# Performance work log

Measured on AMD Instinct MI355X. Metric: run time of the kernel, lower is better.

## Reference

```python
import jax, jax.numpy as jnp
import numpy as np

BLANK = 36
NEG = -1e30  # stand-in for -inf that stays NaN-free under logaddexp


def _ctc_loss(logits, targets, input_lengths, target_lengths):
    """CTC loss (reduction='mean', matching torch.nn.CTCLoss semantics:
    per-sample loss divided by target_length, then mean over batch).
    logits: [B, T, C] raw scores; targets: [B*L] flattened labels (fixed L per sample).
    """
    B, T, C = logits.shape
    L = targets.shape[0] // B
    tgt = targets.reshape(B, L)
    S = 2 * L + 1  # extended label length: blank-interleaved

    # log_softmax over classes, then time-major [T, B, C]
    lp = jnp.transpose(jax.nn.log_softmax(logits, axis=-1), (1, 0, 2))

    # extended targets: [blank, t1, blank, t2, ..., blank]  -> [B, S]
    ext = jnp.full((B, S), BLANK, dtype=tgt.dtype).at[:, 1::2].set(tgt)

    # gather log-probs of extended labels: [T, B, S]
    lp_ext = lp[:, jnp.arange(B)[:, None], ext]

    # positions beyond 2*target_len are invalid
    valid = jnp.arange(S)[None, :] < (2 * target_lengths[:, None] + 1)  # [B, S]
    # skip transition s-2 -> s allowed only if ext[s] != blank and ext[s] != ext[s-2]
    skip_ok = (ext != BLANK) & jnp.concatenate(
        [jnp.zeros((B, 2), bool), ext[:, 2:] != ext[:, :-2]], axis=1)

    end_idx = 2 * target_lengths  # index of final blank; [B]

    def final_ll(alpha):
        e1 = jnp.take_along_axis(alpha, end_idx[:, None], axis=1)[:, 0]
        e2 = jnp.take_along_axis(alpha, (end_idx - 1)[:, None], axis=1)[:, 0]
        return jnp.logaddexp(e1, e2)

    # t = 0 initialization
    alpha0 = jnp.full((B, S), NEG, logits.dtype)
    alpha0 = alpha0.at[:, 0].set(lp_ext[0, :, 0]).at[:, 1].set(lp_ext[0, :, 1])
    alpha0 = jnp.where(valid, alpha0, NEG)
    final0 = jnp.where(input_lengths == 1, final_ll(alpha0), NEG)

    pad1 = jnp.full((B, 1), NEG, logits.dtype)
    pad2 = jnp.full((B, 2), NEG, logits.dtype)

    def step(carry, inp):
        alpha, final = carry
        t, lpe = inp  # lpe: [B, S]
        a1 = jnp.concatenate([pad1, alpha[:, :-1]], axis=1)
        a2 = jnp.where(skip_ok, jnp.concatenate([pad2, alpha[:, :-2]], axis=1), NEG)
        new = jnp.logaddexp(jnp.logaddexp(alpha, a1), a2) + lpe
        new = jnp.where(valid, new, NEG)
        final = jnp.where(input_lengths == t + 1, final_ll(new), final)
        return (new, final), None

    (_, final), _ = jax.lax.scan(step, (alpha0, final0),
                                 (jnp.arange(1, T), lp_ext[1:]))
    return jnp.mean(-final / target_lengths.astype(logits.dtype))


def setup_inputs() -> dict:
    key = jax.random.key(0)
    k1, k2 = jax.random.split(key)
    B, T, C, L = 2048, 256, 37, 16
    logits = jax.random.normal(k1, (B, T, C), dtype=jnp.float32)
    targets = jax.random.randint(k2, (B * L,), 0, 36, dtype=jnp.int32)  # never blank
    input_lengths = jnp.full((B,), T, dtype=jnp.int32)
    target_lengths = jnp.full((B,), L, dtype=jnp.int32)
    return {"logits": logits, "targets": targets,
            "input_lengths": input_lengths, "target_lengths": target_lengths}


def reference(logits, targets, input_lengths, target_lengths):
    return _ctc_loss(logits, targets, input_lengths, target_lengths)
```

## Files before the change

### kernel.cpp

```cpp
#include <hip/hip_runtime.h>

#define BLANK 36
#define NEG -1e30f
#define CC 37
#define LOG32 3.4657359027997265f

__device__ __forceinline__ float logaddexp_f(float a, float b) {
    float m = fmaxf(a, b);
    float d = fabsf(a - b);
    return m + __logf(1.0f + __expf(-d));
}

__global__ __launch_bounds__(256) void ctc_fused_lin_kernel(
    const float* __restrict__ logits,
    const int*   __restrict__ targets,
    const int*   __restrict__ input_lengths,
    const int*   __restrict__ target_lengths,
    float*       __restrict__ per_sample,
    int B, int T, int L)
{
    __shared__ float lds[4 * 4736];
    const int lane = threadIdx.x & 63;
    const int wib  = threadIdx.x >> 6;
    const int b    = blockIdx.x * 4 + wib;
    if (b >= B) return;

    float* X0 = lds + wib * 4736;
    float* X1 = X0 + 2368;

    const int S = 2 * L + 1;
    const int tlen_s = __builtin_amdgcn_readfirstlane(target_lengths[b]);
    const int ilen_s = __builtin_amdgcn_readfirstlane(input_lengths[b]);
    const int end_s  = 2 * tlen_s;

    int ext_s = BLANK;
    if (lane < S && (lane & 1)) ext_s = targets[b * L + (lane >> 1)];
    const int ext_sm2 = __shfl_up(ext_s, 2);
    const bool skip_ok = (lane < S) && (lane >= 2) && (ext_s != BLANK) && (ext_s != ext_sm2);
    const bool valid = lane < (2 * tlen_s + 1);

    const float4* src = (const float4*)(logits + (size_t)b * T * CC);

    float z    = 0.0f;
    float racc = 0.0f;
    float capv = NEG;

    auto ZSTEP = [&](float p, int tt) {
        float z1 = __shfl_up(z, 1);
        z1 = (lane == 0) ? 0.0f : z1;
        float z2 = __shfl_up(z, 2);
        z2 = skip_ok ? z2 : 0.0f;
        const float zn = (z + z1 + z2) * p;
        z = valid ? zn : 0.0f;
        if (ilen_s == tt + 1) {
            capv = __logf(fmaxf(z, 1e-35f)) + racc - (float)(tt + 1) * LOG32;
        }
    };

    auto RESCALE = [&]() {
        float m = z;
        #pragma unroll
        for (int o = 32; o > 0; o >>= 1) m = fmaxf(m, __shfl_xor(m, o));
        m = fmaxf(m, 1e-30f);
        z *= (1.0f / m);
        racc += __logf(m);
    };

    auto SOFTMAX = [&](float* Xn) {
        float xr[CC];
        const float* row = Xn + lane * CC;
        #pragma unroll
        for (int c2 = 0; c2 < CC; ++c2) xr[c2] = row[c2];
        float m = xr[0];
        #pragma unroll
        for (int c2 = 1; c2 < CC; ++c2) m = fmaxf(m, xr[c2]);
        float ss = 0.0f;
        #pragma unroll
        for (int c2 = 0; c2 < CC; ++c2) { xr[c2] = __expf(xr[c2] - m); ss += xr[c2]; }
        const float inv = 32.0f / ss;
        float* wrow = Xn + lane * CC;
        #pragma unroll
        for (int c2 = 0; c2 < CC; ++c2) wrow[c2] = xr[c2] * inv;
    };

    {
        float4* dst = (float4*)X0;
        #pragma unroll
        for (int k = 0; k < 9; ++k) dst[k * 64 + lane] = src[k * 64 + lane];
        if (lane < 16) dst[576 + lane] = src[576 + lane];
        __builtin_amdgcn_s_waitcnt(0);
        SOFTMAX(X0);
        __builtin_amdgcn_s_waitcnt(0);
    }

    const int NC = T >> 6;
    for (int c = 0; c < NC; ++c) {
        float* Xb = (c & 1) ? X1 : X0;
        const bool more = (c + 1 < NC);

        float4 f0 = {}, f1 = {}, f2 = {}, f3 = {}, f4 = {},
               f5 = {}, f6 = {}, f7 = {}, f8 = {}, f9 = {};
        if (more) {
            const float4* s2 = src + (size_t)(c + 1) * 592;
            f0 = s2[lane];       f1 = s2[64 + lane];  f2 = s2[128 + lane];
            f3 = s2[192 + lane]; f4 = s2[256 + lane]; f5 = s2[320 + lane];
            f6 = s2[384 + lane]; f7 = s2[448 + lane]; f8 = s2[512 + lane];
            if (lane < 16) f9 = s2[576 + lane];
        }

        const int tbase = c << 6;
        float p0 = Xb[0 * CC + ext_s];
        float p1 = Xb[1 * CC + ext_s];
        float p2 = Xb[2 * CC + ext_s];
        float p3 = Xb[3 * CC + ext_s];
        float q0, q1, q2, q3;
        int g = 0;
        if (c == 0) {
            z = (valid && lane <= 1) ? p0 : 0.0f;
            if (ilen_s == 1) capv = __logf(fmaxf(z, 1e-35f)) - LOG32;
            q0 = Xb[4 * CC + ext_s];
            q1 = Xb[5 * CC + ext_s];
            q2 = Xb[6 * CC + ext_s];
            q3 = Xb[7 * CC + ext_s];
            ZSTEP(p1, 1); ZSTEP(p2, 2); ZSTEP(p3, 3);
            p0 = q0; p1 = q1; p2 = q2; p3 = q3;
            g = 1;
        }
        for (; g < 16; ++g) {
            const int r = (g + 1) << 2;
            if (g < 15) {
                q0 = Xb[(r + 0) * CC + ext_s];
                q1 = Xb[(r + 1) * CC + ext_s];
                q2 = Xb[(r + 2) * CC + ext_s];
                q3 = Xb[(r + 3) * CC + ext_s];
            }
            const int tt = tbase + (g << 2);
            ZSTEP(p0, tt); ZSTEP(p1, tt + 1); ZSTEP(p2, tt + 2); ZSTEP(p3, tt + 3);
            p0 = q0; p1 = q1; p2 = q2; p3 = q3;
            if (g & 1) RESCALE();
        }

        if (more) {
            float* Xn = (c & 1) ? X0 : X1;
            float4* dst = (float4*)Xn;
            dst[lane] = f0;       dst[64 + lane] = f1;  dst[128 + lane] = f2;
            dst[192 + lane] = f3; dst[256 + lane] = f4; dst[320 + lane] = f5;
            dst[384 + lane] = f6; dst[448 + lane] = f7; dst[512 + lane] = f8;
            if (lane < 16) dst[576 + lane] = f9;
            __builtin_amdgcn_s_waitcnt(0);
            SOFTMAX(Xn);
            __builtin_amdgcn_s_waitcnt(0);
        }
    }

    const float e1 = __shfl(capv, end_s);
    const float e2 = __shfl(capv, end_s - 1);
    const float final_v = logaddexp_f(e1, e2);
    if (lane == 0) per_sample[b] = -final_v / (float)tlen_s;
}

__global__ __launch_bounds__(256) void lse_kernel(
    const float* __restrict__ logits, float* __restrict__ denom, int N)
{
    __shared__ float lds[256 * CC];
    const int lane = threadIdx.x & 63;
    const int wib  = threadIdx.x >> 6;
    const int wave = blockIdx.x * 4 + wib;
    const long long row0 = (long long)wave * 64;
    if (row0 >= N) return;
    const int wbase = wib * 64 * CC;
    const float4* src4 = (const float4*)(logits + row0 * CC);
    const long long n4_remaining = ((long long)N * CC - row0 * CC) / 4;
    float4* lds4 = (float4*)(lds + wbase);
    #pragma unroll
    for (int k = 0; k < 10; ++k) {
        const int idx = k * 64 + lane;
        if (idx < 592 && idx < n4_remaining) lds4[idx] = src4[idx];
    }
    __builtin_amdgcn_s_waitcnt(0);
    const long long row = row0 + lane;
    if (row >= N) return;
    const float* x = lds + wbase + lane * CC;
    float m = x[0];
    #pragma unroll
    for (int c = 1; c < CC; ++c) m = fmaxf(m, x[c]);
    float s = 0.0f;
    #pragma unroll
    for (int c = 0; c < CC; ++c) s += __expf(x[c] - m);
    denom[row] = m + __logf(s);
}

__global__ __launch_bounds__(256) void ctc_alpha2_kernel(
    const float* __restrict__ logits, const float* __restrict__ denom,
    const int* __restrict__ targets, const int* __restrict__ input_lengths,
    const int* __restrict__ target_lengths, float* __restrict__ per_sample,
    int B, int T, int L)
{
    const int wave = (int)((blockIdx.x * blockDim.x + threadIdx.x) >> 6);
    const int lane = threadIdx.x & 63;
    if (wave >= B) return;
    const int b = wave;
    const int S = 2 * L + 1;
    const int tlen = target_lengths[b];
    const int ilen = input_lengths[b];
    const int end_idx = 2 * tlen;
    int ext_s = BLANK;
    if (lane < S && (lane & 1)) ext_s = targets[b * L + (lane >> 1)];
    const int ext_sm2 = __shfl_up(ext_s, 2);
    const bool skip_ok = (lane < S) && (lane >= 2) && (ext_s != BLANK) && (ext_s != ext_sm2);
    const bool valid = lane < (2 * tlen + 1);
    const float* lg = logits + (size_t)b * T * CC;
    const float* dn = denom + (size_t)b * T;
    float x_cur = lg[ext_s];
    float d_cur = dn[0];
    float x_nx = (T > 1) ? lg[CC + ext_s] : 0.0f;
    float d_nx = (T > 1) ? dn[1] : 0.0f;
    float final_v = NEG;
    float alpha = (valid && lane <= 1) ? (x_cur - d_cur) : NEG;
    if (ilen == 1) {
        const float e1 = __shfl(alpha, end_idx);
        const float e2 = __shfl(alpha, end_idx - 1);
        final_v = logaddexp_f(e1, e2);
    }
    for (int tt = 1; tt < T; ++tt) {
        x_cur = x_nx; d_cur = d_nx;
        if (tt + 1 < T) {
            x_nx = lg[(size_t)(tt + 1) * CC + ext_s];
            d_nx = dn[tt + 1];
        }
        const float lpe = x_cur - d_cur;
        float a1 = __shfl_up(alpha, 1);
        if (lane == 0) a1 = NEG;
        float a2 = __shfl_up(alpha, 2);
        if (!skip_ok) a2 = NEG;
        const float m = fmaxf(fmaxf(alpha, a1), a2);
        const float s = __expf(alpha - m) + __expf(a1 - m) + __expf(a2 - m);
        const float na = m + __logf(s) + lpe;
        alpha = valid ? na : NEG;
        if (ilen == tt + 1) {
            const float e1 = __shfl(alpha, end_idx);
            const float e2 = __shfl(alpha, end_idx - 1);
            final_v = logaddexp_f(e1, e2);
        }
    }
    if (lane == 0) per_sample[b] = -final_v / (float)tlen;
}

__global__ __launch_bounds__(256) void ctc_alpha_mono_kernel(
    const float* __restrict__ logits, const int* __restrict__ targets,
    const int* __restrict__ input_lengths, const int* __restrict__ target_lengths,
    float* __restrict__ per_sample, int B, int T, int L)
{
    const int wave = (int)((blockIdx.x * blockDim.x + threadIdx.x) >> 6);
    const int lane = threadIdx.x & 63;
    if (wave >= B) return;
    const int b = wave;
    const int S = 2 * L + 1;
    const int tlen = target_lengths[b];
    const int ilen = input_lengths[b];
    const int end_idx = 2 * tlen;
    int ext_s = BLANK;
    if (lane < S && (lane & 1)) ext_s = targets[b * L + (lane >> 1)];
    const int ext_sm2 = __shfl_up(ext_s, 2);
    const bool skip_ok = (lane < S) && (lane >= 2) && (ext_s != BLANK) && (ext_s != ext_sm2);
    const bool valid = lane < (2 * tlen + 1);
    const float* lg = logits + (size_t)b * T * CC;
    float alpha = NEG, final_v = NEG;
    for (int t = 0; t < T; ++t) {
        float x = (lane < CC) ? lg[t * CC + lane] : -3.0e38f;
        float mx = x;
        #pragma unroll
        for (int o = 32; o > 0; o >>= 1) mx = fmaxf(mx, __shfl_xor(mx, o));
        float e = (lane < CC) ? __expf(x - mx) : 0.0f;
        float se = e;
        #pragma unroll
        for (int o = 32; o > 0; o >>= 1) se += __shfl_xor(se, o);
        const float lp = x - mx - __logf(se);
        const float lpe = __shfl(lp, ext_s);
        float newa;
        if (t == 0) {
            newa = (lane <= 1) ? lpe : NEG;
        } else {
            float a1 = __shfl_up(alpha, 1);
            if (lane == 0) a1 = NEG;
            float a2 = __shfl_up(alpha, 2);
            if (!skip_ok) a2 = NEG;
            newa = logaddexp_f(logaddexp_f(alpha, a1), a2) + lpe;
        }
        if (!valid) newa = NEG;
        alpha = newa;
        if (ilen == t + 1) {
            const float e1 = __shfl(alpha, end_idx);
            const float e2 = __shfl(alpha, end_idx - 1);
            final_v = logaddexp_f(e1, e2);
        }
    }
    if (lane == 0) per_sample[b] = -final_v / (float)tlen;
}

__global__ __launch_bounds__(256) void reduce_mean_kernel(
    const float* __restrict__ ps, float* __restrict__ out, int B)
{
    float s = 0.0f;
    for (int i = threadIdx.x; i < B; i += 256) s += ps[i];
    #pragma unroll
    for (int o = 32; o > 0; o >>= 1) s += __shfl_xor(s, o);
    __shared__ float sm[4];
    const int w = threadIdx.x >> 6, l = threadIdx.x & 63;
    if (l == 0) sm[w] = s;
    __syncthreads();
    if (threadIdx.x == 0) {
        out[0] = (sm[0] + sm[1] + sm[2] + sm[3]) / (float)B;
    }
}

extern "C" void kernel_launch(void* const* d_in, const int* in_sizes, int n_in,
                              void* d_out, int out_size, void* d_ws, size_t ws_size,
                              hipStream_t stream) {
    const float* logits         = (const float*)d_in[0];
    const int*   targets        = (const int*)d_in[1];
    const int*   input_lengths  = (const int*)d_in[2];
    const int*   target_lengths = (const int*)d_in[3];

    const int B = in_sizes[2];
    const int L = in_sizes[1] / B;
    const int T = in_sizes[0] / (B * CC);
    const long long N = (long long)B * T;

    float* per_sample = (float*)d_ws;
    float* scratch    = per_sample + B;
    float* out        = (float*)d_out;

    const size_t ws_mid = ((size_t)B + (size_t)N) * sizeof(float);
    const int nblocks_alpha = (B * 64 + 255) / 256;
    const long long nwaves = (N + 63) / 64;

    if ((T % 64 == 0) && T >= 64 && L <= 31 && ws_size >= (size_t)B * sizeof(float)) {
        ctc_fused_lin_kernel<<<(B + 3) / 4, 256, 0, stream>>>(
            logits, targets, input_lengths, target_lengths, per_sample, B, T, L);
    } else if (ws_size >= ws_mid && T >= 2) {
        lse_kernel<<<(int)((nwaves + 3) / 4), 256, 0, stream>>>(logits, scratch, (int)N);
        ctc_alpha2_kernel<<<nblocks_alpha, 256, 0, stream>>>(
            logits, scratch, targets, input_lengths, target_lengths, per_sample, B, T, L);
    } else {
        ctc_alpha_mono_kernel<<<nblocks_alpha, 256, 0, stream>>>(
            logits, targets, input_lengths, target_lengths, per_sample, B, T, L);
    }
    reduce_mean_kernel<<<1, 256, 0, stream>>>(per_sample, out, B);
}
```

Before: 145.7 us.

## Fuse two CTC alpha time steps per iteration to halve the serial shuffle chain

After: 135.9 us. 1.07x faster.

```diff
diff --git a/kernel.cpp b/kernel.cpp
--- a/kernel.cpp
+++ b/kernel.cpp
@@ -3,7 +3,7 @@
 #define BLANK 36
 #define NEG -1e30f
 #define CC 37
-#define LOG32 3.4657359027997265f
+#define LOG37 3.6109179126442243f
 
 __device__ __forceinline__ float logaddexp_f(float a, float b) {
     float m = fmaxf(a, b);
@@ -11,7 +11,7 @@
     return m + __logf(1.0f + __expf(-d));
 }
 
-__global__ __launch_bounds__(256) void ctc_fused_lin_kernel(
+__global__ __launch_bounds__(256) void ctc_fused_lin2_kernel(
     const float* __restrict__ logits,
     const int*   __restrict__ targets,
     const int*   __restrict__ input_lengths,
@@ -35,26 +35,45 @@
 
     int ext_s = BLANK;
     if (lane < S && (lane & 1)) ext_s = targets[b * L + (lane >> 1)];
-    const int ext_sm2 = __shfl_up(ext_s, 2);
-    const bool skip_ok = (lane < S) && (lane >= 2) && (ext_s != BLANK) && (ext_s != ext_sm2);
-    const bool valid = lane < (2 * tlen_s + 1);
+    const int es1 = __shfl_up(ext_s, 1);
+    const int es2 = __shfl_up(ext_s, 2);
+    const bool skip_ok = (lane < S) && (lane >= 2) && (ext_s != BLANK) && (ext_s != es2);
+    const float kf  = skip_ok ? 1.0f : 0.0f;
+    float k1t = __shfl_up(kf, 1);
+    float k2t = __shfl_up(kf, 2);
+    const float k1f = k1t, k2f = k2t;
+    const float m1f = (lane >= 1) ? 1.0f : 0.0f;
+    const bool  valid  = lane < (2 * tlen_s + 1);
+    const float validm = valid ? 1.0f : 0.0f;
 
     const float4* src = (const float4*)(logits + (size_t)b * T * CC);
 
-    float z    = 0.0f;
-    float racc = 0.0f;
-    float capv = NEG;
-
-    auto ZSTEP = [&](float p, int tt) {
-        float z1 = __shfl_up(z, 1);
-        z1 = (lane == 0) ? 0.0f : z1;
-        float z2 = __shfl_up(z, 2);
-        z2 = skip_ok ? z2 : 0.0f;
-        const float zn = (z + z1 + z2) * p;
-        z = valid ? zn : 0.0f;
-        if (ilen_s == tt + 1) {
-            capv = __logf(fmaxf(z, 1e-35f)) + racc - (float)(tt + 1) * LOG32;
-        }
+    float z = 0.0f, racc = 0.0f, capv = NEG;
+
+    auto PAIR = [&](float Ps, float Pm1, float Pm2, float Qv, int tt) {
+        float a1 = __shfl_up(z, 1); a1 = (lane >= 1) ? a1 : 0.0f;
+        float a2 = __shfl_up(z, 2); a2 = (lane >= 2) ? a2 : 0.0f;
+        float a3 = __shfl_up(z, 3); a3 = (lane >= 3) ? a3 : 0.0f;
+        float a4 = __shfl_up(z, 4); a4 = (lane >= 4) ? a4 : 0.0f;
+        const float G0 = fmaf(kf,  a2, z  + a1);
+        const float G1 = fmaf(k1f, a3, a1 + a2);
+        const float G2 = fmaf(k2f, a4, a2 + a3);
+        const float A1v = Ps * G0;
+        if (ilen_s == tt + 1)
+            capv = __logf(fmaxf(A1v, 1e-35f)) + racc - (float)(tt + 1) * LOG37;
+        float r = fmaf(Pm1, G1, A1v);
+        r = fmaf(Pm2, G2, r);
+        z = Qv * r;
+        if (ilen_s == tt + 2)
+            capv = __logf(fmaxf(z, 1e-35f)) + racc - (float)(tt + 2) * LOG37;
+    };
+
+    auto ZSTEP1 = [&](float Qv, int tt) {
+        float a1 = __shfl_up(z, 1); a1 = (lane >= 1) ? a1 : 0.0f;
+        float a2 = __shfl_up(z, 2); a2 = (lane >= 2) ? a2 : 0.0f;
+        z = fmaf(kf, a2, z + a1) * Qv;
+        if (ilen_s == tt + 1)
+            capv = __logf(fmaxf(z, 1e-35f)) + racc - (float)(tt + 1) * LOG37;
     };
 
     auto RESCALE = [&]() {
@@ -77,7 +96,7 @@
         float ss = 0.0f;
         #pragma unroll
         for (int c2 = 0; c2 < CC; ++c2) { xr[c2] = __expf(xr[c2] - m); ss += xr[c2]; }
-        const float inv = 32.0f / ss;
+        const float inv = 37.0f / ss;
         float* wrow = Xn + lane * CC;
         #pragma unroll
         for (int c2 = 0; c2 < CC; ++c2) wrow[c2] = xr[c2] * inv;
@@ -109,35 +128,49 @@
         }
 
         const int tbase = c << 6;
-        float p0 = Xb[0 * CC + ext_s];
-        float p1 = Xb[1 * CC + ext_s];
-        float p2 = Xb[2 * CC + ext_s];
-        float p3 = Xb[3 * CC + ext_s];
-        float q0, q1, q2, q3;
-        int g = 0;
+        float Ps, Pm1, Pm2, Qv, nPs, nPm1, nPm2, nQv;
         if (c == 0) {
-            z = (valid && lane <= 1) ? p0 : 0.0f;
-            if (ilen_s == 1) capv = __logf(fmaxf(z, 1e-35f)) - LOG32;
-            q0 = Xb[4 * CC + ext_s];
-            q1 = Xb[5 * CC + ext_s];
-            q2 = Xb[6 * CC + ext_s];
-            q3 = Xb[7 * CC + ext_s];
-            ZSTEP(p1, 1); ZSTEP(p2, 2); ZSTEP(p3, 3);
-            p0 = q0; p1 = q1; p2 = q2; p3 = q3;
-            g = 1;
-        }
-        for (; g < 16; ++g) {
-            const int r = (g + 1) << 2;
-            if (g < 15) {
-                q0 = Xb[(r + 0) * CC + ext_s];
-                q1 = Xb[(r + 1) * CC + ext_s];
-                q2 = Xb[(r + 2) * CC + ext_s];
-                q3 = Xb[(r + 3) * CC + ext_s];
+            const float P0 = Xb[ext_s];
+            const float Q1 = Xb[CC + ext_s] * validm;
+            z = ((lane <= 1) ? P0 : 0.0f) * validm;
+            if (ilen_s == 1)
+                capv = __logf(fmaxf(z, 1e-35f)) - LOG37;
+            ZSTEP1(Q1, 1);
+            Ps  = Xb[2 * CC + ext_s];
+            Pm1 = m1f * Xb[2 * CC + es1];
+            Pm2 = kf  * Xb[2 * CC + es2];
+            Qv  = Xb[3 * CC + ext_s] * validm;
+            #pragma unroll
+            for (int g = 0; g < 31; ++g) {
+                if (g < 30) {
+                    const int r = 4 + 2 * g;
+                    nPs  = Xb[r * CC + ext_s];
+                    nPm1 = m1f * Xb[r * CC + es1];
+                    nPm2 = kf  * Xb[r * CC + es2];
+                    nQv  = Xb[(r + 1) * CC + ext_s] * validm;
+                }
+                PAIR(Ps, Pm1, Pm2, Qv, 2 + 2 * g);
+                Ps = nPs; Pm1 = nPm1; Pm2 = nPm2; Qv = nQv;
+                if ((g & 7) == 7 || g == 30) RESCALE();
             }
-            const int tt = tbase + (g << 2);
-            ZSTEP(p0, tt); ZSTEP(p1, tt + 1); ZSTEP(p2, tt + 2); ZSTEP(p3, tt + 3);
-            p0 = q0; p1 = q1; p2 = q2; p3 = q3;
-            if (g & 1) RESCALE();
+        } else {
+            Ps  = Xb[ext_s];
+            Pm1 = m1f * Xb[es1];
+            Pm2 = kf  * Xb[es2];
+            Qv  = Xb[CC + ext_s] * validm;
+            #pragma unroll
+            for (int g = 0; g < 32; ++g) {
+                if (g < 31) {
+                    const int r = 2 + 2 * g;
+                    nPs  = Xb[r * CC + ext_s];
+                    nPm1 = m1f * Xb[r * CC + es1];
+                    nPm2 = kf  * Xb[r * CC + es2];
+                    nQv  = Xb[(r + 1) * CC + ext_s] * validm;
+                }
+                PAIR(Ps, Pm1, Pm2, Qv, tbase + 2 * g);
+                Ps = nPs; Pm1 = nPm1; Pm2 = nPm2; Qv = nQv;
+                if ((g & 7) == 7) RESCALE();
+            }
         }
 
         if (more) {
@@ -336,7 +369,7 @@
     const long long nwaves = (N + 63) / 64;
 
     if ((T % 64 == 0) && T >= 64 && L <= 31 && ws_size >= (size_t)B * sizeof(float)) {
-        ctc_fused_lin_kernel<<<(B + 3) / 4, 256, 0, stream>>>(
+        ctc_fused_lin2_kernel<<<(B + 3) / 4, 256, 0, stream>>>(
             logits, targets, input_lengths, target_lengths, per_sample, B, T, L);
     } else if (ws_size >= ws_mid && T >= 2) {
         lse_kernel<<<(int)((nwaves + 3) / 4), 256, 0, stream>>>(logits, scratch, (int)N);
```
